# Kernel tuning notes

Hardware: AMD Instinct MI355X
Metric: run time of the kernel (lower is better)

The kernel has to match this reference:

```python
import jax, jax.numpy as jnp
import numpy as np

VOCAB = 1024
D = 1024  # predictor_dim
B = 32
U = 512
NULL_INDEX = 0


def setup_inputs() -> dict:
    key = jax.random.key(0)
    ks = jax.random.split(key, 9)
    s = 1.0 / np.sqrt(D)
    return {
        "y": jax.random.randint(ks[0], (B, U), 0, VOCAB, dtype=jnp.int32),
        "embed_table": jax.random.normal(ks[1], (VOCAB, D), jnp.float32) * s,
        "Wx": jax.random.normal(ks[2], (D, 3 * D), jnp.float32) * s,  # input kernel [z|r|h]
        "Wh": jax.random.normal(ks[3], (D, 3 * D), jnp.float32) * s,  # recurrent kernel [z|r|h]
        "bx": jnp.zeros((3 * D,), jnp.float32),  # input bias (reset_after=True)
        "bh": jnp.zeros((3 * D,), jnp.float32),  # recurrent bias (reset_after=True)
        "Wd": jax.random.normal(ks[4], (D, D), jnp.float32) * s,
        "bd": jnp.zeros((D,), jnp.float32),
        "h0": jax.random.normal(ks[5], (D,), jnp.float32),  # self.initial_state
    }


def _gru_scan(tokens, embed_table, Wx, Wh, bx, bh, h0_b):
    # tokens: [B, T] int; returns hidden states [B, T, D]
    x = embed_table[tokens]                       # [B, T, D]
    # Precompute all input projections outside the recurrence (one big GEMM)
    xp = jnp.einsum("btd,de->bte", x, Wx) + bx    # [B, T, 3D]
    xp = jnp.moveaxis(xp, 1, 0)                   # [T, B, 3D]

    def step(h, xp_t):
        hp = h @ Wh + bh                          # [B, 3D], reset_after=True
        xz, xr, xh = jnp.split(xp_t, 3, axis=-1)
        hz, hr, hh = jnp.split(hp, 3, axis=-1)
        z = jax.nn.sigmoid(xz + hz)
        r = jax.nn.sigmoid(xr + hr)
        hcand = jnp.tanh(xh + r * hh)
        h_new = z * h + (1.0 - z) * hcand
        return h_new, h_new

    _, hs = jax.lax.scan(step, h0_b, xp)          # hs: [T, B, D]
    return jnp.moveaxis(hs, 0, 1)                 # [B, T, D]


def reference(y, embed_table, Wx, Wh, bx, bh, Wd, bd, h0):
    Bn = y.shape[0]
    start = jnp.full((Bn, 1), NULL_INDEX, dtype=y.dtype)
    tokens = jnp.concatenate([start, y], axis=1)  # [B, U+1]
    h0_b = jnp.broadcast_to(h0, (Bn, D))
    hs = _gru_scan(tokens, embed_table, Wx, Wh, bx, bh, h0_b)  # [B, U+1, D]
    outs = jnp.einsum("btd,de->bte", hs, Wd) + bd
    return outs
```

## Files before the change

### kernel.cpp

```cpp
#include <hip/hip_runtime.h>
#include <hip/hip_bf16.h>
#include <cstdint>

typedef __bf16 bf16;
typedef __bf16 bf16x8 __attribute__((ext_vector_type(8)));
typedef float  f32x4  __attribute__((ext_vector_type(4)));
typedef uint32_t u32x4 __attribute__((ext_vector_type(4)));

#define D_DIM   1024
#define ND      3072
#define B_SZ    32
#define U_SZ    512
#define T_SZ    513
#define M_REAL  (B_SZ * T_SZ)
#define WXS_LD  1032
#define A_LD    1032

__device__ __forceinline__ f32x4 mfma16(bf16x8 a, bf16x8 b, f32x4 c) {
    return __builtin_amdgcn_mfma_f32_16x16x32_bf16(a, b, c, 0, 0, 0);
}

struct bfpair { bf16x8 hi, lo; };

__device__ __forceinline__ bfpair split8(const float* p) {
    f32x4 a = *(const f32x4*)p;
    f32x4 b = *(const f32x4*)(p + 4);
    bfpair r;
#pragma unroll
    for (int j = 0; j < 4; ++j) {
        r.hi[j] = (bf16)a[j];
        r.lo[j] = (bf16)(a[j] - (float)r.hi[j]);
        r.hi[4 + j] = (bf16)b[j];
        r.lo[4 + j] = (bf16)(b[j] - (float)r.hi[4 + j]);
    }
    return r;
}

__device__ __forceinline__ bf16x8 cvt8(const float* p) {
    f32x4 a = *(const f32x4*)p;
    f32x4 b = *(const f32x4*)(p + 4);
    bf16x8 r;
#pragma unroll
    for (int j = 0; j < 4; ++j) { r[j] = (bf16)a[j]; r[4 + j] = (bf16)b[j]; }
    return r;
}

__device__ __forceinline__ bfpair unpack8(const uint32_t* p) {
    u32x4 a = *(const u32x4*)p;
    u32x4 b = *(const u32x4*)(p + 4);
    union { uint32_t u[4]; bf16x8 v; } H, L;
    H.u[0] = __builtin_amdgcn_perm(a.y, a.x, 0x05040100u);
    H.u[1] = __builtin_amdgcn_perm(a.w, a.z, 0x05040100u);
    H.u[2] = __builtin_amdgcn_perm(b.y, b.x, 0x05040100u);
    H.u[3] = __builtin_amdgcn_perm(b.w, b.z, 0x05040100u);
    L.u[0] = __builtin_amdgcn_perm(a.y, a.x, 0x07060302u);
    L.u[1] = __builtin_amdgcn_perm(a.w, a.z, 0x07060302u);
    L.u[2] = __builtin_amdgcn_perm(b.y, b.x, 0x07060302u);
    L.u[3] = __builtin_amdgcn_perm(b.w, b.z, 0x07060302u);
    bfpair r; r.hi = H.v; r.lo = L.v;
    return r;
}

__global__ void transpose_split(const float* __restrict__ in,
                                bf16* __restrict__ out_hi, bf16* __restrict__ out_lo,
                                int R, int C) {
    __shared__ float tile[32][33];
    const int c0 = blockIdx.x * 32, r0 = blockIdx.y * 32;
    const int tx = threadIdx.x, ty = threadIdx.y;
    for (int i = 0; i < 32; i += 8)
        tile[ty + i][tx] = in[(size_t)(r0 + ty + i) * C + c0 + tx];
    __syncthreads();
    for (int i = 0; i < 32; i += 8) {
        const float v  = tile[tx][ty + i];
        const bf16  hi = (bf16)v;
        out_hi[(size_t)(c0 + ty + i) * R + r0 + tx] = hi;
        out_lo[(size_t)(c0 + ty + i) * R + r0 + tx] = (bf16)(v - (float)hi);
    }
}

__global__ __launch_bounds__(256, 1)
void gru_scan(const float* __restrict__ Wx,    const float* __restrict__ Wh,
              const float* __restrict__ bx,    const float* __restrict__ bh,
              const float* __restrict__ h0,    const float* __restrict__ embed,
              const int* __restrict__ y,       uint32_t* __restrict__ ghs,
              int* __restrict__ flags)
{
    __shared__ __align__(16) bf16 WxS[48 * WXS_LD];
    __shared__ float hpx[48 * 17];
    __shared__ float xpx[2][48 * 17];
    __shared__ float bhs[48], bxs[48];

    const int tid  = threadIdx.x;
    const int wave = tid >> 6, lane = tid & 63;
    const int quad = lane >> 4, l15 = lane & 15;
    const int mhalf = blockIdx.x & 1;
    const int n0 = (blockIdx.x >> 1) * 16;
    const int nblocks = gridDim.x;
    int* cnt = flags;
    int* go  = flags + 512;

    for (int idx = tid; idx < 3 * 1024 * 16; idx += 256) {
        const int cl = idx & 15;
        const int k  = (idx >> 4) & 1023;
        const int g  = idx >> 14;
        WxS[(g * 16 + cl) * WXS_LD + k] = (bf16)Wx[(size_t)k * ND + g * D_DIM + n0 + cl];
    }
    if (tid < 48) {
        bhs[tid] = bh[(tid >> 4) * D_DIM + n0 + (tid & 15)];
        bxs[tid] = bx[(tid >> 4) * D_DIM + n0 + (tid & 15)];
    }

    bf16x8 breg[32];
    if (wave < 3) {
#pragma unroll
        for (int ks = 0; ks < 32; ++ks) {
            bf16x8 v;
#pragma unroll
            for (int j = 0; j < 8; ++j)
                v[j] = (bf16)Wh[(size_t)(ks * 32 + quad * 8 + j) * ND
                                + wave * D_DIM + n0 + l15];
            breg[ks] = v;
        }
    }

    const int gml = tid >> 4, nl = tid & 15;
    const int gb  = mhalf * 16 + gml;
    const int gn  = n0 + nl;
    float hold = h0[gn];
    uint32_t pkjunk = 0;

    __syncthreads();

    if (wave == 3) {
        const float* xrow = embed + quad * 8;
        f32x4 ax0 = {}, ax1 = {}, ax2 = {};
#pragma unroll
        for (int ks = 0; ks < 32; ++ks) {
            bf16x8 xa = cvt8(xrow + ks * 32);
            bf16x8 w0 = *(const bf16x8*)(WxS + (l15)      * WXS_LD + ks * 32 + quad * 8);
            bf16x8 w1 = *(const bf16x8*)(WxS + (16 + l15) * WXS_LD + ks * 32 + quad * 8);
            bf16x8 w2 = *(const bf16x8*)(WxS + (32 + l15) * WXS_LD + ks * 32 + quad * 8);
            ax0 = mfma16(xa, w0, ax0);
            ax1 = mfma16(xa, w1, ax1);
            ax2 = mfma16(xa, w2, ax2);
        }
#pragma unroll
        for (int i = 0; i < 4; ++i) {
            xpx[0][(quad * 4 + i) * 17 + l15]      = ax0[i];
            xpx[0][(16 + quad * 4 + i) * 17 + l15] = ax1[i];
            xpx[0][(32 + quad * 4 + i) * 17 + l15] = ax2[i];
        }
    }

    for (int t = 0; t < T_SZ; ++t) {
        if (wave < 3) {
            f32x4 a0 = {}, a1 = {};
            if (t == 0) {
                const float* hrow = h0 + quad * 8;
#pragma unroll
                for (int ks = 0; ks < 32; ++ks) {
                    bfpair h8 = split8(hrow + ks * 32);
                    a0 = mfma16(h8.hi, breg[ks], a0);
                    a1 = mfma16(h8.lo, breg[ks], a1);
                }
            } else {
                const uint32_t* hrow = ghs
                    + ((size_t)(mhalf * 16 + l15) * T_SZ + (t - 1)) * D_DIM + quad * 8;
#pragma unroll
                for (int ks = 0; ks < 32; ++ks) {
                    bfpair h8 = unpack8(hrow + ks * 32);
                    a0 = mfma16(h8.hi, breg[ks], a0);
                    a1 = mfma16(h8.lo, breg[ks], a1);
                }
            }
            a0 = a0 + a1;
#pragma unroll
            for (int i = 0; i < 4; ++i)
                hpx[(wave * 16 + quad * 4 + i) * 17 + l15] = a0[i];
        }

        if (wave == 3 && t < U_SZ) {
            const int tok = y[(mhalf * 16 + l15) * U_SZ + t] & 1023;
            const float* xrow = embed + (size_t)tok * D_DIM + quad * 8;
            const int p = (t + 1) & 1;
            f32x4 ax0 = {}, ax1 = {}, ax2 = {};
#pragma unroll
            for (int ks = 0; ks < 32; ++ks) {
                bf16x8 xa = cvt8(xrow + ks * 32);
                bf16x8 w0 = *(const bf16x8*)(WxS + (l15)      * WXS_LD + ks * 32 + quad * 8);
                bf16x8 w1 = *(const bf16x8*)(WxS + (16 + l15) * WXS_LD + ks * 32 + quad * 8);
                bf16x8 w2 = *(const bf16x8*)(WxS + (32 + l15) * WXS_LD + ks * 32 + quad * 8);
                ax0 = mfma16(xa, w0, ax0);
                ax1 = mfma16(xa, w1, ax1);
                ax2 = mfma16(xa, w2, ax2);
            }
#pragma unroll
            for (int i = 0; i < 4; ++i) {
                xpx[p][(quad * 4 + i) * 17 + l15]      = ax0[i];
                xpx[p][(16 + quad * 4 + i) * 17 + l15] = ax1[i];
                xpx[p][(32 + quad * 4 + i) * 17 + l15] = ax2[i];
            }
        }
        __syncthreads();

        {
            const int p = t & 1;
            const float xz = xpx[p][(gml)      * 17 + nl] + bxs[nl];
            const float xr = xpx[p][(16 + gml) * 17 + nl] + bxs[16 + nl];
            const float xh = xpx[p][(32 + gml) * 17 + nl] + bxs[32 + nl];
            const float hz = hpx[(gml)      * 17 + nl] + bhs[nl];
            const float hr = hpx[(16 + gml) * 17 + nl] + bhs[16 + nl];
            const float hh = hpx[(32 + gml) * 17 + nl] + bhs[32 + nl];
            const float z  = 1.f / (1.f + __expf(-(xz + hz)));
            const float r  = 1.f / (1.f + __expf(-(xr + hr)));
            const float pa = xh + r * hh;
            const float hc = 1.f - 2.f / (__expf(2.f * pa) + 1.f);
            const float hn = z * hold + (1.f - z) * hc;
            hold = hn;
            union { uint16_t u[2]; uint32_t w; } pk;
            const bf16 hi = (bf16)hn;
            const bf16 lo = (bf16)(hn - (float)hi);
            pk.u[0] = __builtin_bit_cast(uint16_t, hi);
            pk.u[1] = __builtin_bit_cast(uint16_t, lo);
            uint32_t old = __hip_atomic_exchange(
                ghs + ((size_t)gb * T_SZ + t) * D_DIM + gn, pk.w,
                __ATOMIC_RELAXED, __HIP_MEMORY_SCOPE_AGENT);
            pkjunk ^= old;
        }

        if (t + 1 < T_SZ) {
            __syncthreads();
            if (tid == 0) {
                const int c = __hip_atomic_fetch_add(cnt + t, 1, __ATOMIC_RELAXED,
                                                     __HIP_MEMORY_SCOPE_AGENT);
                if (c == nblocks - 1) {
                    __hip_atomic_store(go + t, 1, __ATOMIC_RELAXED,
                                       __HIP_MEMORY_SCOPE_AGENT);
                } else {
                    while (!__hip_atomic_load(go + t, __ATOMIC_RELAXED,
                                              __HIP_MEMORY_SCOPE_AGENT))
                        __builtin_amdgcn_s_sleep(1);
                }
            }
            __syncthreads();
        }
    }

    if (pkjunk == 0xDEADBEEFu) flags[1023] = 1;
}

__global__ __launch_bounds__(256, 1)
void gemm_rows_inplace(float* __restrict__ C,
                       const bf16* __restrict__ WdTh, const bf16* __restrict__ WdTl,
                       const float* __restrict__ bd)
{
    __shared__ __align__(16) bf16 Ah[32 * A_LD];
    __shared__ __align__(16) bf16 Al[32 * A_LD];
    const int tid  = threadIdx.x;
    const int wave = tid >> 6, lane = tid & 63;
    const int quad = lane >> 4, l15 = lane & 15;
    const size_t r0 = (size_t)blockIdx.x * 32;
    const uint32_t* Cw = (const uint32_t*)C;

    for (int idx = tid; idx < 32 * 128; idx += 256) {
        const int r = idx >> 7, ch = idx & 127;
        bfpair p = unpack8(Cw + (r0 + r) * D_DIM + ch * 8);
        *(bf16x8*)(Ah + r * A_LD + ch * 8) = p.hi;
        *(bf16x8*)(Al + r * A_LD + ch * 8) = p.lo;
    }
    __syncthreads();

    f32x4 acc[2][16] = {};
    const int nbase = wave * 256;
    for (int ks = 0; ks < 32; ++ks) {
        bf16x8 a0h = *(const bf16x8*)(Ah + (l15)      * A_LD + ks * 32 + quad * 8);
        bf16x8 a0l = *(const bf16x8*)(Al + (l15)      * A_LD + ks * 32 + quad * 8);
        bf16x8 a1h = *(const bf16x8*)(Ah + (16 + l15) * A_LD + ks * 32 + quad * 8);
        bf16x8 a1l = *(const bf16x8*)(Al + (16 + l15) * A_LD + ks * 32 + quad * 8);
#pragma unroll
        for (int nt = 0; nt < 16; ++nt) {
            const size_t boff = (size_t)(nbase + nt * 16 + l15) * D_DIM + ks * 32 + quad * 8;
            bf16x8 bhv = *(const bf16x8*)(WdTh + boff);
            bf16x8 blv = *(const bf16x8*)(WdTl + boff);
            acc[0][nt] = mfma16(a0h, bhv, acc[0][nt]);
            acc[0][nt] = mfma16(a0l, bhv, acc[0][nt]);
            acc[0][nt] = mfma16(a0h, blv, acc[0][nt]);
            acc[1][nt] = mfma16(a1h, bhv, acc[1][nt]);
            acc[1][nt] = mfma16(a1l, bhv, acc[1][nt]);
            acc[1][nt] = mfma16(a1h, blv, acc[1][nt]);
        }
    }

#pragma unroll
    for (int nt = 0; nt < 16; ++nt) {
        const int col = nbase + nt * 16 + l15;
        const float bvl = bd[col];
#pragma unroll
        for (int mt = 0; mt < 2; ++mt)
#pragma unroll
            for (int i = 0; i < 4; ++i)
                C[(r0 + mt * 16 + quad * 4 + i) * D_DIM + col] =
                    acc[mt][nt][i] + bvl;
    }
}

extern "C" void kernel_launch(void* const* d_in, const int* in_sizes, int n_in,
                              void* d_out, int out_size, void* d_ws, size_t ws_size,
                              hipStream_t stream) {
    (void)in_sizes; (void)n_in; (void)out_size; (void)ws_size;
    const int*   y     = (const int*)  d_in[0];
    const float* embed = (const float*)d_in[1];
    const float* Wx    = (const float*)d_in[2];
    const float* Wh    = (const float*)d_in[3];
    const float* bx    = (const float*)d_in[4];
    const float* bh    = (const float*)d_in[5];
    const float* Wd    = (const float*)d_in[6];
    const float* bd    = (const float*)d_in[7];
    const float* h0    = (const float*)d_in[8];
    float* out = (float*)d_out;

    bf16* WdTh = (bf16*)d_ws;
    bf16* WdTl = WdTh + (size_t)D_DIM * D_DIM;
    int* flags = (int*)((char*)d_ws + (size_t)D_DIM * D_DIM * 4);

    hipMemsetAsync(flags, 0, 8192, stream);

    transpose_split<<<dim3(D_DIM / 32, D_DIM / 32), dim3(32, 8), 0, stream>>>(
        Wd, WdTh, WdTl, D_DIM, D_DIM);

    gru_scan<<<128, 256, 0, stream>>>(Wx, Wh, bx, bh, h0, embed, y,
                                      (uint32_t*)out, flags);

    gemm_rows_inplace<<<M_REAL / 32, 256, 0, stream>>>(out, WdTh, WdTl, bd);
}
```

Before: 7.732 ms.

## Replace atomic counter grid barrier with per-block slots and master-gathered release

Replaces the per-step grid barrier, which used a fetch_add counter plus a go flag, with per-block arrival slots written as monotonic step numbers. Block 0 polls all slots with one wavefront and then releases the others through 8 replicated go flags. Waiting blocks spin without sleep. This aims to remove contention on a single atomic counter and cut release latency, but adds polling traffic and depends on relaxed-ordering visibility of the hidden-state writes.

```diff
diff --git a/kernel.cpp b/kernel.cpp
--- a/kernel.cpp
+++ b/kernel.cpp
@@ -15,6 +15,8 @@
 #define M_REAL  (B_SZ * T_SZ)
 #define WXS_LD  1032
 #define A_LD    1032
+
+#define AGENT __HIP_MEMORY_SCOPE_AGENT
 
 __device__ __forceinline__ f32x4 mfma16(bf16x8 a, bf16x8 b, f32x4 c) {
     return __builtin_amdgcn_mfma_f32_16x16x32_bf16(a, b, c, 0, 0, 0);
@@ -95,9 +97,8 @@
     const int quad = lane >> 4, l15 = lane & 15;
     const int mhalf = blockIdx.x & 1;
     const int n0 = (blockIdx.x >> 1) * 16;
-    const int nblocks = gridDim.x;
-    int* cnt = flags;
-    int* go  = flags + 512;
+    int* slots = flags;
+    int* go    = flags + 512;
 
     for (int idx = tid; idx < 3 * 1024 * 16; idx += 256) {
         const int cl = idx & 15;
@@ -224,22 +225,33 @@
             pk.u[1] = __builtin_bit_cast(uint16_t, lo);
             uint32_t old = __hip_atomic_exchange(
                 ghs + ((size_t)gb * T_SZ + t) * D_DIM + gn, pk.w,
-                __ATOMIC_RELAXED, __HIP_MEMORY_SCOPE_AGENT);
+                __ATOMIC_RELAXED, AGENT);
             pkjunk ^= old;
         }
 
         if (t + 1 < T_SZ) {
             __syncthreads();
-            if (tid == 0) {
-                const int c = __hip_atomic_fetch_add(cnt + t, 1, __ATOMIC_RELAXED,
-                                                     __HIP_MEMORY_SCOPE_AGENT);
-                if (c == nblocks - 1) {
-                    __hip_atomic_store(go + t, 1, __ATOMIC_RELAXED,
-                                       __HIP_MEMORY_SCOPE_AGENT);
-                } else {
-                    while (!__hip_atomic_load(go + t, __ATOMIC_RELAXED,
-                                              __HIP_MEMORY_SCOPE_AGENT))
-                        __builtin_amdgcn_s_sleep(1);
+            const int tv = t + 1;
+            if (blockIdx.x == 0) {
+                if (wave == 0) {
+                    int ok;
+                    do {
+                        const int s1 = __hip_atomic_load(slots + lane * 4,
+                                                         __ATOMIC_RELAXED, AGENT);
+                        const int s2 = __hip_atomic_load(slots + (lane + 64) * 4,
+                                                         __ATOMIC_RELAXED, AGENT);
+                        ok = (lane == 0 || s1 >= tv) && (s2 >= tv);
+                    } while (!__all(ok));
+                    if (lane < 8)
+                        __hip_atomic_store(go + lane * 16, tv,
+                                           __ATOMIC_RELAXED, AGENT);
+                }
+            } else {
+                if (tid == 0) {
+                    __hip_atomic_store(slots + blockIdx.x * 4, tv,
+                                       __ATOMIC_RELAXED, AGENT);
+                    while (__hip_atomic_load(go + (blockIdx.x & 7) * 16,
+                                             __ATOMIC_RELAXED, AGENT) < tv) {}
                 }
             }
             __syncthreads();
```

Measured after the change: 7.591 ms. Within noise of the previous version (-1.8%).
